# Performance work log

Hardware: AMD Instinct MI355X
Metric: run time of the kernel (lower is better)

The kernel has to match this reference:

```python
import jax, jax.numpy as jnp
import numpy as np

N, F, C, B = 500000, 256, 256, 512


def _mlp(x, W1, b1, W2, b2):
    # Linear -> exact GELU -> Linear (matches torch.nn.GELU default)
    return jax.nn.gelu(x @ W1 + b1, approximate=False) @ W2 + b2


def setup_inputs() -> dict:
    key = jax.random.key(0)
    ks = jax.random.split(key, 8)
    s_f = 1.0 / np.sqrt(F)
    s_c = 1.0 / np.sqrt(C)
    x = jax.random.normal(ks[0], (N, F), dtype=jnp.float32)
    u = jax.random.normal(ks[1], (B, C), dtype=jnp.float32)
    batch = jnp.sort(jax.random.randint(ks[2], (N,), 0, B, dtype=jnp.int64))
    return {
        "x": x,
        "u": u,
        "batch": batch,
        "size": B,
        "Wn1": jax.random.normal(ks[3], (F, C), dtype=jnp.float32) * s_f,
        "bn1": jnp.zeros((C,), dtype=jnp.float32),
        "Wn2": jax.random.normal(ks[4], (C, C), dtype=jnp.float32) * s_c,
        "bn2": jnp.zeros((C,), dtype=jnp.float32),
        "Wq1": jax.random.normal(ks[5], (C, C), dtype=jnp.float32) * s_c,
        "bq1": jnp.zeros((C,), dtype=jnp.float32),
        "Wq2": jax.random.normal(ks[6], (C, C), dtype=jnp.float32) * s_c,
        "bq2": jnp.zeros((C,), dtype=jnp.float32),
    }


def reference(x, u, batch, size, Wn1, bn1, Wn2, bn2, Wq1, bq1, Wq2, bq2):
    batch = batch.astype(jnp.int32)
    # node MLP: [N, F] -> [N, C]
    xn = _mlp(x, Wn1, bn1, Wn2, bn2)
    # question MLP: [B, C] -> [B, C], gathered per node
    q = _mlp(u, Wq1, bq1, Wq2, bq2)
    # per-node dot-product gate (bmm of [N,1,C] x [N,C,1]) / sqrt(C)
    gate = jnp.sum(xn * q[batch], axis=-1, keepdims=True) / jnp.sqrt(
        jnp.asarray(xn.shape[1], dtype=xn.dtype))  # [N, 1]
    # segment-wise (per-graph) stable softmax over nodes
    m = jax.ops.segment_max(gate, batch, num_segments=size)  # [B, 1]
    e = jnp.exp(gate - m[batch])
    denom = jax.ops.segment_sum(e, batch, num_segments=size)  # [B, 1]
    gate = e / (denom[batch] + 1e-16)
    # weighted scatter-add pooling: [N, C] -> [B, C]
    out = jax.ops.segment_sum(gate * xn, batch, num_segments=size)
    return out
```

## Files before the change

kernel.cpp:

```cpp
#include <hip/hip_runtime.h>

#define NN 500000
#define CC 256
#define BB 512

typedef __attribute__((ext_vector_type(8))) short short8v;
typedef __attribute__((ext_vector_type(4))) float f32x4;

__device__ __forceinline__ unsigned short f2bf_u(float f){
  unsigned u = __float_as_uint(f);
  unsigned r = u + 0x7FFFu + ((u>>16)&1u);
  return (unsigned short)(r>>16);
}
__device__ __forceinline__ float bf2f(unsigned short h){
  return __uint_as_float(((unsigned)h)<<16);
}
__device__ __forceinline__ float gelu_f(float v){
  return 0.5f*v*(1.0f + erff(v*0.70710678118654752f));
}
__device__ __forceinline__ unsigned encf(float f){
  unsigned u = __float_as_uint(f);
  return (u & 0x80000000u) ? ~u : (u | 0x80000000u);
}
__device__ __forceinline__ float decf(unsigned u){
  return (u & 0x80000000u) ? __uint_as_float(u & 0x7fffffffu) : __uint_as_float(~u);
}

__global__ void qmlp_k(const float* __restrict__ u, const float* __restrict__ Wq1,
                       const float* __restrict__ bq1, const float* __restrict__ Wq2,
                       const float* __restrict__ bq2, float* __restrict__ q){
  __shared__ float us[256];
  __shared__ float hs[256];
  const int row = blockIdx.x, c = threadIdx.x;
  us[c] = u[row*256 + c];
  __syncthreads();
  float s = bq1[c];
  #pragma unroll 4
  for (int k=0;k<256;k++) s = fmaf(us[k], Wq1[k*256+c], s);
  hs[c] = gelu_f(s);
  __syncthreads();
  float s2 = bq2[c];
  #pragma unroll 4
  for (int k=0;k<256;k++) s2 = fmaf(hs[k], Wq2[k*256+c], s2);
  q[row*256+c] = s2;
}

__global__ void wtrans_k(const float* __restrict__ Wn1, const float* __restrict__ Wn2,
                         unsigned short* __restrict__ W1T, unsigned short* __restrict__ W2T){
  const float* W = blockIdx.y ? Wn2 : Wn1;
  unsigned short* T = blockIdx.y ? W2T : W1T;
  const int k = blockIdx.x, c = threadIdx.x;
  T[c*256 + k] = f2bf_u(W[k*256 + c]);
}

template<int PASS>
__global__ void __launch_bounds__(256)
mlp_gemm(const float* __restrict__ xin, const unsigned short* __restrict__ hin,
         const unsigned short* __restrict__ WT, const float* __restrict__ bias,
         unsigned short* __restrict__ hout, const float* __restrict__ q,
         const int* __restrict__ batch, float* __restrict__ gate){
  __shared__ unsigned short Ald[64*64];
  __shared__ unsigned short Bld[256*64];
  const int t = threadIdx.x;
  const int bid = blockIdx.x;
  const int rowbase = bid*64;
  const int w = t>>6, l = t&63;
  const int lg = l>>4, li = l&15;
  const int wc = w;

  f32x4 acc[4][4];
  const f32x4 zero = {0.f,0.f,0.f,0.f};
  #pragma unroll
  for (int m=0;m<4;m++)
    #pragma unroll
    for (int n=0;n<4;n++) acc[m][n] = zero;

  const int arow = t>>2, acq = t&3;
  int gr = rowbase + arow; if (gr >= NN) gr = NN-1;

  for (int kk=0; kk<256; kk+=64){
    if (PASS==1){
      const float4* src = (const float4*)(xin + (size_t)gr*256 + kk + acq*16);
      float4 f0=src[0], f1=src[1], f2=src[2], f3=src[3];
      uint4 o0, o1;
      o0.x = (unsigned)f2bf_u(f0.x) | ((unsigned)f2bf_u(f0.y)<<16);
      o0.y = (unsigned)f2bf_u(f0.z) | ((unsigned)f2bf_u(f0.w)<<16);
      o0.z = (unsigned)f2bf_u(f1.x) | ((unsigned)f2bf_u(f1.y)<<16);
      o0.w = (unsigned)f2bf_u(f1.z) | ((unsigned)f2bf_u(f1.w)<<16);
      o1.x = (unsigned)f2bf_u(f2.x) | ((unsigned)f2bf_u(f2.y)<<16);
      o1.y = (unsigned)f2bf_u(f2.z) | ((unsigned)f2bf_u(f2.w)<<16);
      o1.z = (unsigned)f2bf_u(f3.x) | ((unsigned)f2bf_u(f3.y)<<16);
      o1.w = (unsigned)f2bf_u(f3.z) | ((unsigned)f2bf_u(f3.w)<<16);
      uint4* dst = (uint4*)(Ald + arow*64 + acq*16);
      dst[0]=o0; dst[1]=o1;
    } else {
      const uint4* src = (const uint4*)(hin + (size_t)gr*256 + kk + acq*16);
      uint4 v0=src[0], v1=src[1];
      uint4* dst = (uint4*)(Ald + arow*64 + acq*16);
      dst[0]=v0; dst[1]=v1;
    }
    {
      const uint4* src = (const uint4*)(WT + (size_t)t*256 + kk);
      uint4* dst = (uint4*)(Bld + t*64);
      #pragma unroll
      for (int i=0;i<8;i++) dst[i] = src[i];
    }
    __syncthreads();
    const unsigned short* ab = Ald + li*64 + lg*8;
    const unsigned short* bb = Bld + (wc*64 + li)*64 + lg*8;
    #pragma unroll
    for (int ks=0; ks<64; ks+=32){
      short8v a[4], b[4];
      #pragma unroll
      for (int m=0;m<4;m++) a[m] = *(const short8v*)(ab + m*1024 + ks);
      #pragma unroll
      for (int n=0;n<4;n++) b[n] = *(const short8v*)(bb + n*1024 + ks);
      #pragma unroll
      for (int m=0;m<4;m++)
        #pragma unroll
        for (int n=0;n<4;n++)
          acc[m][n] = __builtin_amdgcn_mfma_f32_16x16x32_bf16(a[m], b[n], acc[m][n], 0, 0, 0);
    }
    __syncthreads();
  }

  if (PASS==1){
    #pragma unroll
    for (int m=0;m<4;m++){
      #pragma unroll
      for (int n=0;n<4;n++){
        const int gcol = wc*64 + n*16 + li;
        const float bs = bias[gcol];
        f32x4 v = acc[m][n];
        #pragma unroll
        for (int r=0;r<4;r++){
          const int grow = rowbase + m*16 + lg*4 + r;
          if (grow < NN)
            hout[(size_t)grow*256 + gcol] = f2bf_u(gelu_f(v[r]+bs));
        }
      }
    }
  } else {
    #pragma unroll
    for (int m=0;m<4;m++){
      int grows[4], bsg[4];
      #pragma unroll
      for (int r=0;r<4;r++){
        grows[r] = rowbase + m*16 + lg*4 + r;
        bsg[r] = (grows[r] < NN) ? batch[grows[r]] : 0;
      }
      float p[4] = {0.f,0.f,0.f,0.f};
      #pragma unroll
      for (int n=0;n<4;n++){
        const int gcol = wc*64 + n*16 + li;
        const float bs = bias[gcol];
        f32x4 v = acc[m][n];
        #pragma unroll
        for (int r=0;r<4;r++){
          if (grows[r] < NN){
            const float val = v[r] + bs;
            hout[(size_t)grows[r]*256 + gcol] = f2bf_u(val);
            p[r] = fmaf(val, q[bsg[r]*256 + gcol], p[r]);
          }
        }
      }
      #pragma unroll
      for (int r=0;r<4;r++){
        float pr = p[r];
        pr += __shfl_xor(pr, 1);
        pr += __shfl_xor(pr, 2);
        pr += __shfl_xor(pr, 4);
        pr += __shfl_xor(pr, 8);
        if (li==0 && grows[r] < NN) atomicAdd(gate + grows[r], pr*0.0625f);
      }
    }
  }
}

__global__ void segmax_k(const float* __restrict__ gate, const int* __restrict__ batch,
                         unsigned* __restrict__ menc){
  const int i = blockIdx.x*512 + threadIdx.x;
  const bool ok = i < NN;
  const int b = ok ? batch[i] : batch[NN-1];
  unsigned e = encf(ok ? gate[i] : -3.4e38f);
  const int b0 = __shfl(b, 0), b63 = __shfl(b, 63);
  if (b0 == b63){
    #pragma unroll
    for (int off=32; off; off>>=1){ unsigned o = __shfl_xor(e, off); e = e > o ? e : o; }
    if ((threadIdx.x & 63) == 0) atomicMax(menc + b, e);
  } else {
    atomicMax(menc + b, e);
  }
}

__global__ void expden_k(float* __restrict__ gate, const int* __restrict__ batch,
                         const unsigned* __restrict__ menc, float* __restrict__ denom){
  const int i = blockIdx.x*512 + threadIdx.x;
  const bool ok = i < NN;
  const int b = ok ? batch[i] : batch[NN-1];
  const float mm = decf(menc[b]);
  float e = ok ? expf(gate[i] - mm) : 0.f;
  if (ok) gate[i] = e;
  const int b0 = __shfl(b, 0), b63 = __shfl(b, 63);
  if (b0 == b63){
    float s = e;
    #pragma unroll
    for (int off=32; off; off>>=1) s += __shfl_xor(s, off);
    if ((threadIdx.x & 63) == 0) atomicAdd(denom + b, s);
  } else {
    atomicAdd(denom + b, e);
  }
}

__global__ void pool_k(const unsigned short* __restrict__ xn, const float* __restrict__ e,
                       const float* __restrict__ denom, const int* __restrict__ batch,
                       float* __restrict__ out){
  const int wid = blockIdx.x*4 + (threadIdx.x>>6);
  const int l = threadIdx.x & 63;
  const int NW = gridDim.x*4;
  const int per = (NN + NW - 1)/NW;
  const int n0 = wid*per;
  if (n0 >= NN) return;
  int n1 = n0 + per; if (n1 > NN) n1 = NN;

  float a0=0.f, a1=0.f, a2=0.f, a3=0.f;
  int bcur = batch[n0];
  float invd = 1.0f/(denom[bcur] + 1e-16f);
  for (int n=n0; n<n1; ++n){
    const int b = batch[n];
    if (b != bcur){
      float* o = out + bcur*256 + l*4;
      atomicAdd(o+0, a0); atomicAdd(o+1, a1); atomicAdd(o+2, a2); atomicAdd(o+3, a3);
      a0=a1=a2=a3=0.f;
      bcur = b;
      invd = 1.0f/(denom[bcur] + 1e-16f);
    }
    const float wgt = e[n]*invd;
    const ushort4 xv = *(const ushort4*)(xn + (size_t)n*256 + l*4);
    a0 = fmaf(wgt, bf2f(xv.x), a0);
    a1 = fmaf(wgt, bf2f(xv.y), a1);
    a2 = fmaf(wgt, bf2f(xv.z), a2);
    a3 = fmaf(wgt, bf2f(xv.w), a3);
  }
  float* o = out + bcur*256 + l*4;
  atomicAdd(o+0, a0); atomicAdd(o+1, a1); atomicAdd(o+2, a2); atomicAdd(o+3, a3);
}

extern "C" void kernel_launch(void* const* d_in, const int* in_sizes, int n_in,
                              void* d_out, int out_size, void* d_ws, size_t ws_size,
                              hipStream_t stream){
  const float* x   = (const float*)d_in[0];
  const float* u   = (const float*)d_in[1];
  const int*  batch= (const int*)d_in[2];
  const float* Wn1 = (const float*)d_in[4];
  const float* bn1 = (const float*)d_in[5];
  const float* Wn2 = (const float*)d_in[6];
  const float* bn2 = (const float*)d_in[7];
  const float* Wq1 = (const float*)d_in[8];
  const float* bq1 = (const float*)d_in[9];
  const float* Wq2 = (const float*)d_in[10];
  const float* bq2 = (const float*)d_in[11];
  float* out = (float*)d_out;

  char* ws = (char*)d_ws;
  unsigned short* hws = (unsigned short*)ws;
  float* gate          = (float*)(ws + 256000000);
  float* q             = (float*)(ws + 258000000);
  unsigned short* W1T  = (unsigned short*)(ws + 258524288);
  unsigned short* W2T  = (unsigned short*)(ws + 258655360);
  unsigned* menc       = (unsigned*)(ws + 258786432);
  float* denom         = (float*)(ws + 258788480);

  hipMemsetAsync(gate, 0, (size_t)NN*4, stream);
  hipMemsetAsync(menc, 0, BB*4, stream);
  hipMemsetAsync(denom, 0, BB*4, stream);
  hipMemsetAsync(out, 0, (size_t)BB*CC*4, stream);

  qmlp_k<<<BB, 256, 0, stream>>>(u, Wq1, bq1, Wq2, bq2, q);
  wtrans_k<<<dim3(256,2), 256, 0, stream>>>(Wn1, Wn2, W1T, W2T);

  const int gblocks = (NN + 63)/64;
  mlp_gemm<1><<<gblocks, 256, 0, stream>>>(x, nullptr, W1T, bn1, hws,
                                           nullptr, nullptr, nullptr);
  mlp_gemm<2><<<gblocks, 256, 0, stream>>>(nullptr, hws, W2T, bn2, hws,
                                           q, batch, gate);

  segmax_k<<<(NN+511)/512, 512, 0, stream>>>(gate, batch, menc);
  expden_k<<<(NN+511)/512, 512, 0, stream>>>(gate, batch, menc, denom);
  pool_k<<<1024, 256, 0, stream>>>(hws, gate, denom, batch, out);
}
```

Before: 1.545 ms.

## Enlarge GEMM tile to 128 rows with k-chunked LDS layout

The node-MLP GEMM now uses 512-thread blocks covering 128 rows instead of 64, arranged as a 2x4 wave grid, so each staged weight tile is reused across twice as many rows. The weights are pre-packed into a k-chunk-of-8 interleaved layout, and LDS tiles for A and B use a matching layout so MFMA operand reads are contiguous and likely suffer fewer bank conflicts. The pool kernel grid is also doubled. In exchange, LDS use and register pressure per block go up. The in-place aliasing of hin and hout also loses its restrict qualifiers.

```diff
diff --git a/kernel.cpp b/kernel.cpp
--- a/kernel.cpp
+++ b/kernel.cpp
@@ -45,28 +45,27 @@
   q[row*256+c] = s2;
 }
 
-__global__ void wtrans_k(const float* __restrict__ Wn1, const float* __restrict__ Wn2,
-                         unsigned short* __restrict__ W1T, unsigned short* __restrict__ W2T){
+__global__ void wk_k(const float* __restrict__ Wn1, const float* __restrict__ Wn2,
+                     unsigned short* __restrict__ Wk1, unsigned short* __restrict__ Wk2){
   const float* W = blockIdx.y ? Wn2 : Wn1;
-  unsigned short* T = blockIdx.y ? W2T : W1T;
+  unsigned short* T = blockIdx.y ? Wk2 : Wk1;
   const int k = blockIdx.x, c = threadIdx.x;
-  T[c*256 + k] = f2bf_u(W[k*256 + c]);
+  T[(k>>3)*2048 + c*8 + (k&7)] = f2bf_u(W[k*256 + c]);
 }
 
 template<int PASS>
-__global__ void __launch_bounds__(256)
-mlp_gemm(const float* __restrict__ xin, const unsigned short* __restrict__ hin,
-         const unsigned short* __restrict__ WT, const float* __restrict__ bias,
-         unsigned short* __restrict__ hout, const float* __restrict__ q,
+__global__ void __launch_bounds__(512, 4)
+mlp_gemm(const float* __restrict__ xin, const unsigned short* hin,
+         const unsigned short* __restrict__ Wk, const float* __restrict__ bias,
+         unsigned short* hout, const float* __restrict__ q,
          const int* __restrict__ batch, float* __restrict__ gate){
-  __shared__ unsigned short Ald[64*64];
-  __shared__ unsigned short Bld[256*64];
+  __shared__ unsigned short Asw[8*128*8];
+  __shared__ unsigned short Bsw[8*256*8];
   const int t = threadIdx.x;
-  const int bid = blockIdx.x;
-  const int rowbase = bid*64;
+  const int rowbase = blockIdx.x*128;
   const int w = t>>6, l = t&63;
   const int lg = l>>4, li = l&15;
-  const int wc = w;
+  const int wr = w>>2, wc = w&3;
 
   f32x4 acc[4][4];
   const f32x4 zero = {0.f,0.f,0.f,0.f};
@@ -75,12 +74,12 @@
     #pragma unroll
     for (int n=0;n<4;n++) acc[m][n] = zero;
 
-  const int arow = t>>2, acq = t&3;
-  int gr = rowbase + arow; if (gr >= NN) gr = NN-1;
+  const int ar = t>>2, ac = t&3;
+  int gr = rowbase + ar; if (gr >= NN) gr = NN-1;
 
   for (int kk=0; kk<256; kk+=64){
     if (PASS==1){
-      const float4* src = (const float4*)(xin + (size_t)gr*256 + kk + acq*16);
+      const float4* src = (const float4*)(xin + (size_t)gr*256 + kk + ac*16);
       float4 f0=src[0], f1=src[1], f2=src[2], f3=src[3];
       uint4 o0, o1;
       o0.x = (unsigned)f2bf_u(f0.x) | ((unsigned)f2bf_u(f0.y)<<16);
@@ -91,30 +90,32 @@
       o1.y = (unsigned)f2bf_u(f2.z) | ((unsigned)f2bf_u(f2.w)<<16);
       o1.z = (unsigned)f2bf_u(f3.x) | ((unsigned)f2bf_u(f3.y)<<16);
       o1.w = (unsigned)f2bf_u(f3.z) | ((unsigned)f2bf_u(f3.w)<<16);
-      uint4* dst = (uint4*)(Ald + arow*64 + acq*16);
-      dst[0]=o0; dst[1]=o1;
+      *(uint4*)(Asw + (2*ac+0)*1024 + ar*8) = o0;
+      *(uint4*)(Asw + (2*ac+1)*1024 + ar*8) = o1;
     } else {
-      const uint4* src = (const uint4*)(hin + (size_t)gr*256 + kk + acq*16);
+      const uint4* src = (const uint4*)(hin + (size_t)gr*256 + kk + ac*16);
       uint4 v0=src[0], v1=src[1];
-      uint4* dst = (uint4*)(Ald + arow*64 + acq*16);
-      dst[0]=v0; dst[1]=v1;
+      *(uint4*)(Asw + (2*ac+0)*1024 + ar*8) = v0;
+      *(uint4*)(Asw + (2*ac+1)*1024 + ar*8) = v1;
     }
     {
-      const uint4* src = (const uint4*)(WT + (size_t)t*256 + kk);
-      uint4* dst = (uint4*)(Bld + t*64);
-      #pragma unroll
-      for (int i=0;i<8;i++) dst[i] = src[i];
+      const unsigned short* wsrc = Wk + kk*256;
+      #pragma unroll
+      for (int i=0;i<4;i++){
+        const int g = i*512 + t;
+        *(uint4*)(Bsw + g*8) = *(const uint4*)(wsrc + g*8);
+      }
     }
     __syncthreads();
-    const unsigned short* ab = Ald + li*64 + lg*8;
-    const unsigned short* bb = Bld + (wc*64 + li)*64 + lg*8;
-    #pragma unroll
-    for (int ks=0; ks<64; ks+=32){
+    const unsigned short* Ab = Asw + lg*1024 + (wr*64 + li)*8;
+    const unsigned short* Bb = Bsw + lg*2048 + (wc*64 + li)*8;
+    #pragma unroll
+    for (int ksc=0; ksc<8; ksc+=4){
       short8v a[4], b[4];
       #pragma unroll
-      for (int m=0;m<4;m++) a[m] = *(const short8v*)(ab + m*1024 + ks);
-      #pragma unroll
-      for (int n=0;n<4;n++) b[n] = *(const short8v*)(bb + n*1024 + ks);
+      for (int m=0;m<4;m++) a[m] = *(const short8v*)(Ab + ksc*1024 + m*128);
+      #pragma unroll
+      for (int n=0;n<4;n++) b[n] = *(const short8v*)(Bb + ksc*2048 + n*128);
       #pragma unroll
       for (int m=0;m<4;m++)
         #pragma unroll
@@ -124,6 +125,7 @@
     __syncthreads();
   }
 
+  const int rw0 = rowbase + wr*64;
   if (PASS==1){
     #pragma unroll
     for (int m=0;m<4;m++){
@@ -134,7 +136,7 @@
         f32x4 v = acc[m][n];
         #pragma unroll
         for (int r=0;r<4;r++){
-          const int grow = rowbase + m*16 + lg*4 + r;
+          const int grow = rw0 + m*16 + lg*4 + r;
           if (grow < NN)
             hout[(size_t)grow*256 + gcol] = f2bf_u(gelu_f(v[r]+bs));
         }
@@ -146,7 +148,7 @@
       int grows[4], bsg[4];
       #pragma unroll
       for (int r=0;r<4;r++){
-        grows[r] = rowbase + m*16 + lg*4 + r;
+        grows[r] = rw0 + m*16 + lg*4 + r;
         bsg[r] = (grows[r] < NN) ? batch[grows[r]] : 0;
       }
       float p[4] = {0.f,0.f,0.f,0.f};
@@ -266,8 +268,8 @@
   unsigned short* hws = (unsigned short*)ws;
   float* gate          = (float*)(ws + 256000000);
   float* q             = (float*)(ws + 258000000);
-  unsigned short* W1T  = (unsigned short*)(ws + 258524288);
-  unsigned short* W2T  = (unsigned short*)(ws + 258655360);
+  unsigned short* Wk1  = (unsigned short*)(ws + 258524288);
+  unsigned short* Wk2  = (unsigned short*)(ws + 258655360);
   unsigned* menc       = (unsigned*)(ws + 258786432);
   float* denom         = (float*)(ws + 258788480);
 
@@ -277,15 +279,15 @@
   hipMemsetAsync(out, 0, (size_t)BB*CC*4, stream);
 
   qmlp_k<<<BB, 256, 0, stream>>>(u, Wq1, bq1, Wq2, bq2, q);
-  wtrans_k<<<dim3(256,2), 256, 0, stream>>>(Wn1, Wn2, W1T, W2T);
-
-  const int gblocks = (NN + 63)/64;
-  mlp_gemm<1><<<gblocks, 256, 0, stream>>>(x, nullptr, W1T, bn1, hws,
+  wk_k<<<dim3(256,2), 256, 0, stream>>>(Wn1, Wn2, Wk1, Wk2);
+
+  const int gblocks = (NN + 127)/128;
+  mlp_gemm<1><<<gblocks, 512, 0, stream>>>(x, nullptr, Wk1, bn1, hws,
                                            nullptr, nullptr, nullptr);
-  mlp_gemm<2><<<gblocks, 256, 0, stream>>>(nullptr, hws, W2T, bn2, hws,
+  mlp_gemm<2><<<gblocks, 512, 0, stream>>>(nullptr, hws, Wk2, bn2, hws,
                                            q, batch, gate);
 
   segmax_k<<<(NN+511)/512, 512, 0, stream>>>(gate, batch, menc);
   expden_k<<<(NN+511)/512, 512, 0, stream>>>(gate, batch, menc, denom);
-  pool_k<<<1024, 256, 0, stream>>>(hws, gate, denom, batch, out);
-}
+  pool_k<<<2048, 256, 0, stream>>>(hws, gate, denom, batch, out);
+}
```

New measurement: 1.284 ms. 16.9% less time.
